# Kernel tuning notes

Hardware: AMD Instinct MI355X
Metric: run time of the kernel (lower is better)

Reference implementation:

```python
import jax, jax.numpy as jnp
import numpy as np

HIDDEN = 2048
HEADS = 16
HEAD_DIM = HIDDEN // HEADS
THETA = 10000.0


def _rope(x, seq_len):
    # x: [B, S, H, Dh]; standard rotate-half RoPE (cos1==cos2, sin1==sin2 in source)
    d = x.shape[-1]
    inv_freq = 1.0 / (THETA ** (jnp.arange(0, d, 2, dtype=jnp.float32) / d))  # [Dh/2]
    freqs = jnp.arange(seq_len, dtype=jnp.float32)[:, None] * inv_freq[None, :]  # [S, Dh/2]
    cos = jnp.cos(freqs)[None, :, None, :]  # [1,S,1,Dh/2]
    sin = jnp.sin(freqs)[None, :, None, :]
    x1, x2 = x[..., : d // 2], x[..., d // 2 :]
    return jnp.concatenate([x1 * cos - x2 * sin, x1 * sin + x2 * cos], axis=-1)


def setup_inputs() -> dict:
    key = jax.random.key(0)
    ks = jax.random.split(key, 5)
    B, S = 2, 2048
    scale = 1.0 / np.sqrt(HIDDEN)
    return {
        "x": jax.random.normal(ks[0], (B, S, HIDDEN), dtype=jnp.float32),
        "Wq": jax.random.normal(ks[1], (HIDDEN, HIDDEN), dtype=jnp.float32) * scale,
        "Wk": jax.random.normal(ks[2], (HIDDEN, HIDDEN), dtype=jnp.float32) * scale,
        "Wv": jax.random.normal(ks[3], (HIDDEN, HIDDEN), dtype=jnp.float32) * scale,
        "Wo": jax.random.normal(ks[4], (HIDDEN, HIDDEN), dtype=jnp.float32) * scale,
    }


def reference(x, Wq, Wk, Wv, Wo):
    B, S, _ = x.shape
    # nn.Linear(bias=False): y = x @ W.T
    q = (x @ Wq.T).reshape(B, S, HEADS, HEAD_DIM)
    k = (x @ Wk.T).reshape(B, S, HEADS, HEAD_DIM)
    v = (x @ Wv.T).reshape(B, S, HEADS, HEAD_DIM)
    q = _rope(q, S)
    k = _rope(k, S)
    # [B,H,S,S] scores
    scores = jnp.einsum("bqhd,bkhd->bhqk", q, k) / jnp.sqrt(jnp.float32(HEAD_DIM))
    attn = jax.nn.softmax(scores, axis=-1)
    out = jnp.einsum("bhqk,bkhd->bqhd", attn, v).reshape(B, S, HIDDEN)
    return out @ Wo.T
```

## Files before the change

kernel.cpp:

```cpp
#include <hip/hip_runtime.h>
#include <hip/hip_bf16.h>


typedef __attribute__((ext_vector_type(8))) short short8;
typedef __attribute__((ext_vector_type(4))) float f32x4;
typedef __attribute__((ext_vector_type(4))) unsigned short us4;
typedef __attribute__((ext_vector_type(4))) unsigned int u32x4;

__device__ __forceinline__ void gll16(const void* g, void* l) {
  __builtin_amdgcn_global_load_lds((const __attribute__((address_space(1))) void*)g,
                                   (__attribute__((address_space(3))) void*)l, 16, 0, 0);
}

__device__ __forceinline__ unsigned short f2bf(float f) {
  __hip_bfloat16 h = __float2bfloat16(f);
  return *reinterpret_cast<unsigned short*>(&h);
}

__device__ __forceinline__ float bf2f(short s) {
  union { unsigned int u; float f; } c;
  c.u = ((unsigned int)(unsigned short)s) << 16;
  return c.f;
}

__device__ __forceinline__ unsigned int cvtpk(float lo, float hi) {
  unsigned int r;
  asm("v_cvt_pk_bf16_f32 %0, %1, %2" : "=v"(r) : "v"(lo), "v"(hi));
  return r;
}

__global__ __launch_bounds__(256) void cast_f32_bf16(const float* __restrict__ in,
                                                     __hip_bfloat16* __restrict__ out, int n4) {
  int i = blockIdx.x * 256 + threadIdx.x;
  if (i >= n4) return;
  const float4 v = reinterpret_cast<const float4*>(in)[i];
  us4 o;
  o[0] = f2bf(v.x); o[1] = f2bf(v.y); o[2] = f2bf(v.z); o[3] = f2bf(v.w);
  *reinterpret_cast<us4*>(out + (size_t)i * 4) = o;
}

__global__ __launch_bounds__(256) void cast3_w(const float* __restrict__ wq,
                                               const float* __restrict__ wk,
                                               const float* __restrict__ wv,
                                               __hip_bfloat16* __restrict__ dq,
                                               __hip_bfloat16* __restrict__ dk,
                                               __hip_bfloat16* __restrict__ dv, int n4) {
  int i = blockIdx.x * 256 + threadIdx.x;
  const float* in;
  __hip_bfloat16* out;
  int j = i;
  if (i < n4) { in = wq; out = dq; }
  else if (i < 2 * n4) { in = wk; out = dk; j = i - n4; }
  else if (i < 3 * n4) { in = wv; out = dv; j = i - 2 * n4; }
  else return;
  const float4 v = reinterpret_cast<const float4*>(in)[j];
  us4 o;
  o[0] = f2bf(v.x); o[1] = f2bf(v.y); o[2] = f2bf(v.z); o[3] = f2bf(v.w);
  *reinterpret_cast<us4*>(out + (size_t)j * 4) = o;
}

template <typename EPI>
__device__ __forceinline__ void gemm_core(const __hip_bfloat16* A, const __hip_bfloat16* Bt,
                                          int row0, int col0, int K, EPI epi) {
  __shared__ char As[2][16384];
  __shared__ char Bs[2][16384];
  const int tid = threadIdx.x;
  const int lane = tid & 63, wid = tid >> 6;
  const int l15 = lane & 15, l4 = lane >> 4;
  const int wm = (wid >> 1) * 64, wn = (wid & 1) * 64;

  f32x4 acc[4][4] = {};

  const int rs = lane >> 3;
  const int cs = lane & 7;
  const int cg = cs ^ rs;
  const char* Ab = (const char*)A;
  const char* Bb = (const char*)Bt;
  const size_t Kb = (size_t)K * 2;
  const int NT = K >> 6;

#define GSTAGE(T, S)                                                                      \
  {                                                                                       \
    const int k0_ = (T) << 6;                                                             \
    _Pragma("unroll") for (int c_ = 0; c_ < 4; ++c_) {                                    \
      const int cid_ = wid * 4 + c_;                                                      \
      const int r_ = cid_ * 8 + rs;                                                       \
      gll16(Ab + (size_t)(row0 + r_) * Kb + (size_t)k0_ * 2 + cg * 16, As[S] + cid_ * 1024); \
      gll16(Bb + (size_t)(col0 + r_) * Kb + (size_t)k0_ * 2 + cg * 16, Bs[S] + cid_ * 1024); \
    }                                                                                     \
  }

  GSTAGE(0, 0);
  GSTAGE(1, 1);
  asm volatile("s_waitcnt vmcnt(8)" ::: "memory");
  __builtin_amdgcn_s_barrier();

  for (int t = 0; t < NT; ++t) {
    const int s = t & 1;
    short8 a[2][4], b[2][4];
#pragma unroll
    for (int kc = 0; kc < 2; ++kc)
#pragma unroll
      for (int i = 0; i < 4; ++i) {
        const int ra = wm + i * 16 + l15;
        a[kc][i] = *(const short8*)(As[s] + ra * 128 + (((kc * 4 + l4) ^ (ra & 7)) * 16));
        const int rb = wn + i * 16 + l15;
        b[kc][i] = *(const short8*)(Bs[s] + rb * 128 + (((kc * 4 + l4) ^ (rb & 7)) * 16));
      }
    asm volatile("s_waitcnt lgkmcnt(0)" ::: "memory");
    __builtin_amdgcn_sched_barrier(0);
    __builtin_amdgcn_s_barrier();
    if (t + 2 < NT) {
      GSTAGE(t + 2, s);
      asm volatile("s_waitcnt vmcnt(8)" ::: "memory");
    } else if (t + 2 == NT) {
      asm volatile("s_waitcnt vmcnt(0)" ::: "memory");
    }
    __builtin_amdgcn_s_barrier();
#pragma unroll
    for (int kc = 0; kc < 2; ++kc) {
      __builtin_amdgcn_s_setprio(1);
#pragma unroll
      for (int i = 0; i < 4; ++i)
#pragma unroll
        for (int j = 0; j < 4; ++j)
          acc[i][j] = __builtin_amdgcn_mfma_f32_16x16x32_bf16(a[kc][i], b[kc][j], acc[i][j], 0, 0, 0);
      __builtin_amdgcn_s_setprio(0);
    }
  }
  epi(acc, wm, wn, l15, l4);
#undef GSTAGE
}

template <int MODE>
__global__ __launch_bounds__(256) void gemm_bt(const __hip_bfloat16* __restrict__ A,
                                               const __hip_bfloat16* __restrict__ Bt,
                                               void* __restrict__ Cout,
                                               int M, int N, int K) {
  const int row0 = blockIdx.x * 128, col0 = blockIdx.y * 128;
  gemm_core(A, Bt, row0, col0, K, [=](f32x4 (&acc)[4][4], int wm, int wn, int l15, int l4) {
    if (MODE == 2) {
      __hip_bfloat16* vt = (__hip_bfloat16*)Cout;
#pragma unroll
      for (int i = 0; i < 4; ++i) {
        const int gm = row0 + wm + i * 16 + l4 * 4;
        const int bb = gm >> 11, kvb = gm & 2047;
        const int phys = (kvb & ~31) + (((kvb >> 2) & 3) << 3) + (((kvb >> 4) & 1) << 2);
#pragma unroll
        for (int j = 0; j < 4; ++j) {
          const int gn = col0 + wn + j * 16 + l15;
          const int h = gn >> 7, d = gn & 127;
          us4 o;
          o[0] = f2bf(acc[i][j][0]); o[1] = f2bf(acc[i][j][1]);
          o[2] = f2bf(acc[i][j][2]); o[3] = f2bf(acc[i][j][3]);
          *reinterpret_cast<us4*>(vt + ((size_t)((bb * 16 + h) * 128 + d) * 2048 + phys)) = o;
        }
      }
    } else {
#pragma unroll
      for (int i = 0; i < 4; ++i)
#pragma unroll
        for (int j = 0; j < 4; ++j) {
          const int gn = col0 + wn + j * 16 + l15;
#pragma unroll
          for (int r = 0; r < 4; ++r) {
            const int gm = row0 + wm + i * 16 + l4 * 4 + r;
            if (MODE == 0)
              ((__hip_bfloat16*)Cout)[(size_t)gm * N + gn] = __float2bfloat16(acc[i][j][r]);
            else
              ((float*)Cout)[(size_t)gm * N + gn] = acc[i][j][r];
          }
        }
    }
  });
}

__global__ __launch_bounds__(256) void gemm_qkv(const __hip_bfloat16* __restrict__ A,
                                                const __hip_bfloat16* __restrict__ Wq,
                                                const __hip_bfloat16* __restrict__ Wk,
                                                const __hip_bfloat16* __restrict__ Wv,
                                                __hip_bfloat16* __restrict__ qb,
                                                __hip_bfloat16* __restrict__ kb,
                                                __hip_bfloat16* __restrict__ vtb) {
  const int row0 = blockIdx.x * 128;
  const int By = blockIdx.y;
  const int sel = By >> 4;
  const int col0 = (By & 15) * 128;
  const __hip_bfloat16* Bt = (sel == 0) ? Wq : (sel == 1) ? Wk : Wv;
  __hip_bfloat16* outq = (sel == 0) ? qb : kb;

  gemm_core(A, Bt, row0, col0, 2048, [=](f32x4 (&acc)[4][4], int wm, int wn, int l15, int l4) {
    if (sel == 2) {
#pragma unroll
      for (int i = 0; i < 4; ++i) {
        const int gm = row0 + wm + i * 16 + l4 * 4;
        const int bb = gm >> 11, kvb = gm & 2047;
        const int phys = (kvb & ~31) + (((kvb >> 2) & 3) << 3) + (((kvb >> 4) & 1) << 2);
#pragma unroll
        for (int j = 0; j < 4; ++j) {
          const int gn = col0 + wn + j * 16 + l15;
          const int h = gn >> 7, d = gn & 127;
          us4 o;
          o[0] = f2bf(acc[i][j][0]); o[1] = f2bf(acc[i][j][1]);
          o[2] = f2bf(acc[i][j][2]); o[3] = f2bf(acc[i][j][3]);
          *reinterpret_cast<us4*>(vtb + ((size_t)((bb * 16 + h) * 128 + d) * 2048 + phys)) = o;
        }
      }
    } else {
#pragma unroll
      for (int i = 0; i < 4; ++i)
#pragma unroll
        for (int j = 0; j < 4; ++j) {
          const int gn = col0 + wn + j * 16 + l15;
#pragma unroll
          for (int r = 0; r < 4; ++r) {
            const int gm = row0 + wm + i * 16 + l4 * 4 + r;
            outq[(size_t)gm * 2048 + gn] = __float2bfloat16(acc[i][j][r]);
          }
        }
    }
  });
}

__global__ __launch_bounds__(256) void rope_k(__hip_bfloat16* __restrict__ q,
                                              __hip_bfloat16* __restrict__ k) {
  const int tid = blockIdx.x * 256 + threadIdx.x;
  const int i8 = tid & 7;
  const int h = (tid >> 3) & 15;
  const int row = (tid >> 7) & 4095;
  __hip_bfloat16* p = (tid >> 19) ? k : q;
  const int pos = row & 2047;
  const size_t base = (size_t)row * 2048 + h * 128 + i8 * 8;
  const short8 v1 = *reinterpret_cast<const short8*>(p + base);
  const short8 v2 = *reinterpret_cast<const short8*>(p + base + 64);
  short8 o1, o2;
#pragma unroll
  for (int j = 0; j < 8; ++j) {
    const int i = i8 * 8 + j;
    const float invf = exp2f((float)i * -0.20762050593046f);
    const float fr = (float)pos * invf;
    float sv, cv;
    sincosf(fr, &sv, &cv);
    const float x1 = bf2f(v1[j]), x2 = bf2f(v2[j]);
    o1[j] = (short)f2bf(x1 * cv - x2 * sv);
    o2[j] = (short)f2bf(x1 * sv + x2 * cv);
  }
  *reinterpret_cast<short8*>(p + base) = o1;
  *reinterpret_cast<short8*>(p + base + 64) = o2;
}

__global__ __launch_bounds__(256) void flash_k(const __hip_bfloat16* __restrict__ q,
                                               const __hip_bfloat16* __restrict__ k,
                                               const __hip_bfloat16* __restrict__ vt,
                                               __hip_bfloat16* __restrict__ ao) {
  __shared__ char Ks[2][16384];
  __shared__ char VTs[2][16384];
  const int tid = threadIdx.x, lane = tid & 63, wid = tid >> 6;
  const int bx = blockIdx.x;
  const int qt = bx >> 5, bh = bx & 31, b = bh >> 4, h = bh & 15;
  const int l15 = lane & 15, l4 = lane >> 4;

  short8 qf[2][4];
  const char* qB = (const char*)q;
#pragma unroll
  for (int mi = 0; mi < 2; ++mi)
#pragma unroll
    for (int kc = 0; kc < 4; ++kc) {
      const size_t off =
          ((size_t)(b * 2048 + qt * 128 + wid * 32 + mi * 16 + l15) * 2048 + h * 128 + kc * 32 + l4 * 8) * 2;
      qf[mi][kc] = *(const short8*)(qB + off);
    }

  f32x4 oacc[2][8] = {};
  float lr[2] = {0.f, 0.f};

  const char* kbase = (const char*)k + ((size_t)(b * 2048) * 2048 + h * 128) * 2;
  const char* vtbase = (const char*)vt + ((size_t)bh * 128 * 2048) * 2;
  const float SC2 = 0.1275224187f;

  const int krow = lane >> 4, kcol = lane & 15;
  const int vrow = lane >> 3, vcol = lane & 7;
  u32x4 kreg[4], vreg[4];
  int kaddr[4], vaddr[4];
#pragma unroll
  for (int c = 0; c < 4; ++c) {
    const int cid = wid * 4 + c;
    const int rk = cid * 4 + krow;
    kaddr[c] = cid * 1024 + krow * 256 + ((kcol ^ (rk & 7)) * 16);
    const int rv = cid * 8 + vrow;
    vaddr[c] = cid * 1024 + vrow * 128 + ((vcol ^ (rv & 7)) * 16);
  }

#define KVLOAD(T)                                                                             \
  {                                                                                           \
    const int kv0_ = (T)*64;                                                                  \
    _Pragma("unroll") for (int c_ = 0; c_ < 4; ++c_) {                                        \
      const int cid_ = wid * 4 + c_;                                                          \
      kreg[c_] = *(const u32x4*)(kbase + (size_t)(kv0_ + cid_ * 4 + krow) * 4096 + kcol * 16);\
      vreg[c_] = *(const u32x4*)(vtbase + (size_t)(cid_ * 8 + vrow) * 4096 +                  \
                                 (size_t)kv0_ * 2 + vcol * 16);                               \
    }                                                                                         \
  }
#define KVWRITE(BUF)                                                                          \
  {                                                                                           \
    _Pragma("unroll") for (int c_ = 0; c_ < 4; ++c_) {                                        \
      *(u32x4*)(Ks[BUF] + kaddr[c_]) = kreg[c_];                                              \
      *(u32x4*)(VTs[BUF] + vaddr[c_]) = vreg[c_];                                             \
    }                                                                                         \
  }

  KVLOAD(0);
  KVWRITE(0);
  __syncthreads();
  int cur = 0;

  for (int t = 0; t < 32; ++t) {
    if (t < 31) KVLOAD(t + 1);

    f32x4 sacc[2][4] = {};
#pragma unroll
    for (int kc = 0; kc < 4; ++kc) {
      short8 kf[4];
#pragma unroll
      for (int ni = 0; ni < 4; ++ni) {
        const int r = ni * 16 + l15;
        kf[ni] = *(const short8*)(Ks[cur] + r * 256 + (((kc * 4 + l4) ^ (r & 7)) * 16));
      }
#pragma unroll
      for (int mi = 0; mi < 2; ++mi)
#pragma unroll
        for (int ni = 0; ni < 4; ++ni)
          sacc[mi][ni] = __builtin_amdgcn_mfma_f32_16x16x32_bf16(kf[ni], qf[mi][kc], sacc[mi][ni], 0, 0, 0);
    }

    unsigned int W[2][4][2];
#pragma unroll
    for (int mi = 0; mi < 2; ++mi) {
      float rs = 0.f;
#pragma unroll
      for (int ni = 0; ni < 4; ++ni) {
        float p0 = exp2f(sacc[mi][ni][0] * SC2);
        float p1 = exp2f(sacc[mi][ni][1] * SC2);
        float p2 = exp2f(sacc[mi][ni][2] * SC2);
        float p3 = exp2f(sacc[mi][ni][3] * SC2);
        rs += (p0 + p1) + (p2 + p3);
        W[mi][ni][0] = cvtpk(p0, p1);
        W[mi][ni][1] = cvtpk(p2, p3);
      }
      rs += __shfl_xor(rs, 16);
      rs += __shfl_xor(rs, 32);
      lr[mi] += rs;
    }

#pragma unroll
    for (int kc = 0; kc < 2; ++kc) {
      union { u32x4 u; short8 s; } pfu[2];
#pragma unroll
      for (int mi = 0; mi < 2; ++mi) {
        pfu[mi].u[0] = W[mi][kc * 2][0];
        pfu[mi].u[1] = W[mi][kc * 2][1];
        pfu[mi].u[2] = W[mi][kc * 2 + 1][0];
        pfu[mi].u[3] = W[mi][kc * 2 + 1][1];
      }
#pragma unroll
      for (int nd = 0; nd < 8; ++nd) {
        const int r = nd * 16 + l15;
        const short8 vf = *(const short8*)(
            VTs[cur] + r * 128 + (((kc * 4 + l4) ^ (r & 7)) * 16));
#pragma unroll
        for (int mi = 0; mi < 2; ++mi)
          oacc[mi][nd] = __builtin_amdgcn_mfma_f32_16x16x32_bf16(vf, pfu[mi].s, oacc[mi][nd], 0, 0, 0);
      }
    }

    if (t < 31) KVWRITE(cur ^ 1);
    __syncthreads();
    cur ^= 1;
  }

#pragma unroll
  for (int mi = 0; mi < 2; ++mi) {
    const float inv = 1.f / lr[mi];
    const int qrow = qt * 128 + wid * 32 + mi * 16 + l15;
    const size_t rowoff = ((size_t)(b * 2048 + qrow)) * 2048 + h * 128;
#pragma unroll
    for (int nd = 0; nd < 8; ++nd) {
      us4 o;
      o[0] = f2bf(oacc[mi][nd][0] * inv);
      o[1] = f2bf(oacc[mi][nd][1] * inv);
      o[2] = f2bf(oacc[mi][nd][2] * inv);
      o[3] = f2bf(oacc[mi][nd][3] * inv);
      *reinterpret_cast<us4*>(ao + rowoff + nd * 16 + l4 * 4) = o;
    }
  }
#undef KVLOAD
#undef KVWRITE
}

extern "C" void kernel_launch(void* const* d_in, const int* in_sizes, int n_in,
                              void* d_out, int out_size, void* d_ws, size_t ws_size,
                              hipStream_t stream) {
  const float* x  = (const float*)d_in[0];
  const float* Wq = (const float*)d_in[1];
  const float* Wk = (const float*)d_in[2];
  const float* Wv = (const float*)d_in[3];
  const float* Wo = (const float*)d_in[4];
  float* out = (float*)d_out;

  const size_t MK = (size_t)4096 * 2048;
  const size_t WN = (size_t)2048 * 2048;
  if (ws_size < (4 * MK + WN) * 2) return;

  __hip_bfloat16* ws  = (__hip_bfloat16*)d_ws;
  __hip_bfloat16* xb  = ws;
  __hip_bfloat16* qb  = ws + MK;
  __hip_bfloat16* kb  = ws + 2 * MK;
  __hip_bfloat16* vtb = ws + 3 * MK;
  __hip_bfloat16* wsl = ws + 4 * MK;
  __hip_bfloat16* aob = xb;
  __hip_bfloat16* dk = (__hip_bfloat16*)d_out;
  __hip_bfloat16* dv = dk + WN;

  const dim3 gW((int)(WN / 4 / 256));
  const dim3 gX((int)(MK / 4 / 256));

  cast_f32_bf16<<<gX, 256, 0, stream>>>(x, xb, (int)(MK / 4));
  cast3_w<<<dim3((int)(3 * WN / 4 / 256)), 256, 0, stream>>>(Wq, Wk, Wv, wsl, dk, dv,
                                                             (int)(WN / 4));
  gemm_qkv<<<dim3(32, 48), 256, 0, stream>>>(xb, wsl, dk, dv, qb, kb, vtb);
  rope_k<<<4096, 256, 0, stream>>>(qb, kb);
  flash_k<<<512, 256, 0, stream>>>(qb, kb, vtb, aob);
  cast_f32_bf16<<<gW, 256, 0, stream>>>(Wo, wsl, (int)(WN / 4));
  gemm_bt<1><<<dim3(32, 16), 256, 0, stream>>>(aob, wsl, out, 4096, 2048, 2048);
}
```

Before: 266.8 us.

## Stage K/V tiles via direct global-to-LDS loads with two-ahead prefetch

Replaces the register-staged K/V load-then-store double buffering in the attention loop with global_load_lds DMA directly into LDS. Swizzling moves to the global address side. Prefetch now runs two tiles ahead, with explicit vmcnt waits and raw s_barrier calls. This removes the VGPRs held for staging and the LDS write instructions, and aims to overlap memory traffic with the MFMA work more fully. In exchange it relies on hand-managed waitcnt/barrier sequencing, and it reads global memory with a permuted column order instead of storing to LDS with a permuted order.

```diff
diff --git a/kernel.cpp b/kernel.cpp
--- a/kernel.cpp
+++ b/kernel.cpp
@@ -280,42 +280,28 @@
 
   const int krow = lane >> 4, kcol = lane & 15;
   const int vrow = lane >> 3, vcol = lane & 7;
-  u32x4 kreg[4], vreg[4];
-  int kaddr[4], vaddr[4];
-#pragma unroll
-  for (int c = 0; c < 4; ++c) {
-    const int cid = wid * 4 + c;
-    const int rk = cid * 4 + krow;
-    kaddr[c] = cid * 1024 + krow * 256 + ((kcol ^ (rk & 7)) * 16);
-    const int rv = cid * 8 + vrow;
-    vaddr[c] = cid * 1024 + vrow * 128 + ((vcol ^ (rv & 7)) * 16);
-  }
-
-#define KVLOAD(T)                                                                             \
+
+#define GSTAGE(T, S)                                                                          \
   {                                                                                           \
     const int kv0_ = (T)*64;                                                                  \
     _Pragma("unroll") for (int c_ = 0; c_ < 4; ++c_) {                                        \
       const int cid_ = wid * 4 + c_;                                                          \
-      kreg[c_] = *(const u32x4*)(kbase + (size_t)(kv0_ + cid_ * 4 + krow) * 4096 + kcol * 16);\
-      vreg[c_] = *(const u32x4*)(vtbase + (size_t)(cid_ * 8 + vrow) * 4096 +                  \
-                                 (size_t)kv0_ * 2 + vcol * 16);                               \
+      const int rk_ = cid_ * 4 + krow;                                                        \
+      gll16(kbase + (size_t)(kv0_ + rk_) * 4096 + ((kcol ^ (rk_ & 7)) * 16),                  \
+            Ks[S] + cid_ * 1024);                                                             \
+      const int rv_ = cid_ * 8 + vrow;                                                        \
+      gll16(vtbase + (size_t)rv_ * 4096 + (size_t)kv0_ * 2 + ((vcol ^ (rv_ & 7)) * 16),       \
+            VTs[S] + cid_ * 1024);                                                            \
     }                                                                                         \
   }
-#define KVWRITE(BUF)                                                                          \
-  {                                                                                           \
-    _Pragma("unroll") for (int c_ = 0; c_ < 4; ++c_) {                                        \
-      *(u32x4*)(Ks[BUF] + kaddr[c_]) = kreg[c_];                                              \
-      *(u32x4*)(VTs[BUF] + vaddr[c_]) = vreg[c_];                                             \
-    }                                                                                         \
-  }
-
-  KVLOAD(0);
-  KVWRITE(0);
-  __syncthreads();
-  int cur = 0;
+
+  GSTAGE(0, 0);
+  GSTAGE(1, 1);
+  asm volatile("s_waitcnt vmcnt(8)" ::: "memory");
+  __builtin_amdgcn_s_barrier();
 
   for (int t = 0; t < 32; ++t) {
-    if (t < 31) KVLOAD(t + 1);
+    const int s = t & 1;
 
     f32x4 sacc[2][4] = {};
 #pragma unroll
@@ -324,7 +310,7 @@
 #pragma unroll
       for (int ni = 0; ni < 4; ++ni) {
         const int r = ni * 16 + l15;
-        kf[ni] = *(const short8*)(Ks[cur] + r * 256 + (((kc * 4 + l4) ^ (r & 7)) * 16));
+        kf[ni] = *(const short8*)(Ks[s] + r * 256 + (((kc * 4 + l4) ^ (r & 7)) * 16));
       }
 #pragma unroll
       for (int mi = 0; mi < 2; ++mi)
@@ -366,16 +352,23 @@
       for (int nd = 0; nd < 8; ++nd) {
         const int r = nd * 16 + l15;
         const short8 vf = *(const short8*)(
-            VTs[cur] + r * 128 + (((kc * 4 + l4) ^ (r & 7)) * 16));
+            VTs[s] + r * 128 + (((kc * 4 + l4) ^ (r & 7)) * 16));
 #pragma unroll
         for (int mi = 0; mi < 2; ++mi)
           oacc[mi][nd] = __builtin_amdgcn_mfma_f32_16x16x32_bf16(vf, pfu[mi].s, oacc[mi][nd], 0, 0, 0);
       }
     }
 
-    if (t < 31) KVWRITE(cur ^ 1);
-    __syncthreads();
-    cur ^= 1;
+    asm volatile("s_waitcnt lgkmcnt(0)" ::: "memory");
+    __builtin_amdgcn_sched_barrier(0);
+    __builtin_amdgcn_s_barrier();
+    if (t + 2 < 32) {
+      GSTAGE(t + 2, s);
+      asm volatile("s_waitcnt vmcnt(8)" ::: "memory");
+    } else if (t + 2 == 32) {
+      asm volatile("s_waitcnt vmcnt(0)" ::: "memory");
+    }
+    __builtin_amdgcn_s_barrier();
   }
 
 #pragma unroll
@@ -393,8 +386,7 @@
       *reinterpret_cast<us4*>(ao + rowoff + nd * 16 + l4 * 4) = o;
     }
   }
-#undef KVLOAD
-#undef KVWRITE
+#undef GSTAGE
 }
 
 extern "C" void kernel_launch(void* const* d_in, const int* in_sizes, int n_in,
```

After: 266.8 us. Within noise of the previous version (-0.0%).
